# Kernel optimization log

Hardware: AMD Instinct MI355X
Metric: run time of the kernel (lower is better)

## Reference

```python
import jax, jax.numpy as jnp
import numpy as np

B, N, E, H = 1, 4096, 256, 4
D = E // H  # 64


def setup_inputs() -> dict:
    key = jax.random.key(0)
    ks = jax.random.split(key, 16)
    s = lambda fan_in: 1.0 / np.sqrt(fan_in)
    inp = {
        "x": jax.random.normal(ks[0], (B, N, E), dtype=jnp.float32),
        "encoding": jax.random.normal(ks[1], (2, 1, 1, N, D), dtype=jnp.float32),
        # Wqkv: Linear(E, 3E)
        "Wqkv_w": jax.random.uniform(ks[2], (3 * E, E), jnp.float32, -s(E), s(E)),
        "Wqkv_b": jax.random.uniform(ks[3], (3 * E,), jnp.float32, -s(E), s(E)),
        # out_proj: Linear(E, E)
        "out_w": jax.random.uniform(ks[4], (E, E), jnp.float32, -s(E), s(E)),
        "out_b": jax.random.uniform(ks[5], (E,), jnp.float32, -s(E), s(E)),
        # ffn[0]: Linear(2E, 2E)
        "ffn1_w": jax.random.uniform(ks[6], (2 * E, 2 * E), jnp.float32, -s(2 * E), s(2 * E)),
        "ffn1_b": jax.random.uniform(ks[7], (2 * E,), jnp.float32, -s(2 * E), s(2 * E)),
        # ffn[1]: LayerNorm(2E)
        "ln_g": jnp.ones((2 * E,), jnp.float32),
        "ln_b": jnp.zeros((2 * E,), jnp.float32),
        # ffn[3]: Linear(2E, E)
        "ffn2_w": jax.random.uniform(ks[8], (E, 2 * E), jnp.float32, -s(2 * E), s(2 * E)),
        "ffn2_b": jax.random.uniform(ks[9], (E,), jnp.float32, -s(2 * E), s(2 * E)),
    }
    return inp


def _rotate_half(t):
    # t: (B, H, N, D) -> pairwise rotate along last dim
    t2 = t.reshape(B, H, -1, D // 2, 2)
    t2 = jnp.stack((-t2[..., 1], t2[..., 0]), axis=-1)
    return t2.reshape(B, H, -1, D)


def _layernorm(x, g, b, eps=1e-5):
    mu = jnp.mean(x, axis=-1, keepdims=True)
    var = jnp.mean(jnp.square(x - mu), axis=-1, keepdims=True)
    return (x - mu) * jax.lax.rsqrt(var + eps) * g + b


def reference(x, encoding, Wqkv_w, Wqkv_b, out_w, out_b,
              ffn1_w, ffn1_b, ln_g, ln_b, ffn2_w, ffn2_b):
    # fused QKV projection; last dim layout is (H, D, 3)
    qkv = x @ Wqkv_w.T + Wqkv_b                       # (B, N, 3E)
    qkv = qkv.reshape(B, N, H, D, 3).transpose(0, 2, 1, 3, 4)  # (B, H, N, D, 3)
    q, k, v = qkv[..., 0], qkv[..., 1], qkv[..., 2]
    # cached rotary embedding: t*cos + rotate_half(t)*sin
    q = q * encoding[0] + _rotate_half(q) * encoding[1]
    k = k * encoding[0] + _rotate_half(k) * encoding[1]
    # scaled dot-product attention (no mask)
    scores = jnp.einsum("bhqd,bhkd->bhqk", q, k) / np.sqrt(D).astype(np.float32)
    probs = jax.nn.softmax(scores, axis=-1)
    ctx = jnp.einsum("bhqk,bhkd->bhqd", probs, v)     # (B, H, N, D)
    ctx = ctx.transpose(0, 2, 1, 3).reshape(B, N, E)
    message = ctx @ out_w.T + out_b
    # concat-FFN with residual
    h = jnp.concatenate((x, message), axis=-1)        # (B, N, 2E)
    h = h @ ffn1_w.T + ffn1_b
    h = _layernorm(h, ln_g, ln_b)
    h = jax.nn.gelu(h, approximate=False)
    h = h @ ffn2_w.T + ffn2_b
    return x + h
```

## Files before the change

### kernel.cpp

```cpp
#include <hip/hip_runtime.h>
#include <math.h>

#define NTOK 4096
#define EMB  256
#define NH   4
#define HD   64

typedef unsigned short u16;
typedef __attribute__((ext_vector_type(8))) __bf16 bf16x8;
typedef __attribute__((ext_vector_type(4))) float f32x4;

__device__ __forceinline__ u16 f2bf(float f) {
    union { float f; unsigned u; } v; v.f = f;
    unsigned b = v.u;
    b += 0x7FFFu + ((b >> 16) & 1u);
    return (u16)(b >> 16);
}
__device__ __forceinline__ float bf2f(u16 u) {
    union { unsigned u; float f; } v; v.u = ((unsigned)u) << 16;
    return v.f;
}

__global__ __launch_bounds__(256) void w4cast(
    const float4* __restrict__ w0, const float4* __restrict__ w1,
    const float4* __restrict__ w2, const float4* __restrict__ w3,
    u16* __restrict__ dst)
{
    const int f = blockIdx.x * 256 + threadIdx.x;
    float4 v;
    if      (f <  49152) v = w0[f];
    else if (f <  65536) v = w1[f - 49152];
    else if (f < 131072) v = w2[f - 65536];
    else                 v = w3[f - 131072];
    uint2 o;
    o.x = (unsigned)f2bf(v.x) | ((unsigned)f2bf(v.y) << 16);
    o.y = (unsigned)f2bf(v.z) | ((unsigned)f2bf(v.w) << 16);
    *(uint2*)(dst + (size_t)f * 4) = o;
}

__global__ __launch_bounds__(256) void xcast(
    const float4* __restrict__ x4, u16* __restrict__ xb, u16* __restrict__ catb)
{
    const int f = blockIdx.x * 256 + threadIdx.x;
    float4 v = x4[f];
    uint2 o;
    o.x = (unsigned)f2bf(v.x) | ((unsigned)f2bf(v.y) << 16);
    o.y = (unsigned)f2bf(v.z) | ((unsigned)f2bf(v.w) << 16);
    *(uint2*)(xb + (size_t)f * 4) = o;
    const int row = f >> 6, c = (f & 63) * 4;
    *(uint2*)(catb + (size_t)row * 512 + c) = o;
}

__global__ __launch_bounds__(256) void gemm_bf16_abt(
    const u16* __restrict__ A,
    const u16* __restrict__ B,
    const float* __restrict__ bias,
    const float* __restrict__ resid, int ldr,
    float* __restrict__ Cf, u16* __restrict__ Cb, int ldc, int K)
{
    const int t = threadIdx.x, w = t >> 6, l = t & 63;
    const int lg = l >> 4, li = l & 15;
    const int row0 = blockIdx.y * 64 + w * 16;
    const int col0 = blockIdx.x * 64;

    f32x4 acc[4];
    #pragma unroll
    for (int nb = 0; nb < 4; ++nb) acc[nb] = (f32x4){0.f, 0.f, 0.f, 0.f};

    const u16* Ap = A + (size_t)(row0 + li) * K + lg * 8;
    const u16* Bp = B + (size_t)(col0 + li) * K + lg * 8;

    #pragma unroll 2
    for (int k0 = 0; k0 < K; k0 += 32) {
        bf16x8 a = *(const bf16x8*)(Ap + k0);
        #pragma unroll
        for (int nb = 0; nb < 4; ++nb) {
            bf16x8 b = *(const bf16x8*)(Bp + (size_t)nb * 16 * K + k0);
            acc[nb] = __builtin_amdgcn_mfma_f32_16x16x32_bf16(a, b, acc[nb], 0, 0, 0);
        }
    }

    #pragma unroll
    for (int nb = 0; nb < 4; ++nb) {
        const int col = col0 + nb * 16 + li;
        const float bs = bias[col];
        #pragma unroll
        for (int p = 0; p < 4; ++p) {
            const int row = row0 + lg * 4 + p;
            float v = acc[nb][p] + bs;
            if (resid) v += resid[(size_t)row * ldr + col];
            if (Cf) Cf[(size_t)row * ldc + col] = v;
            else    Cb[(size_t)row * ldc + col] = f2bf(v);
        }
    }
}

__global__ __launch_bounds__(256) void rope_qk(
    const u16* __restrict__ qkvb, const float* __restrict__ enc,
    unsigned* __restrict__ Qb, unsigned* __restrict__ Kb)
{
    const int gid = blockIdx.x * 256 + threadIdx.x;
    const int h   = gid >> 17;
    const int rem = gid & (NTOK * 32 - 1);
    const int n   = rem >> 5;
    const int p   = rem & 31;
    const int d0  = p * 2;

    const u16* base = qkvb + (size_t)n * 768 + h * 192 + d0 * 3;
    const float q0v = bf2f(base[0]), k0 = bf2f(base[1]);
    const float q1  = bf2f(base[3]), k1 = bf2f(base[4]);

    float2 c01 = *(const float2*)(enc + (size_t)n * 64 + d0);
    float2 s01 = *(const float2*)(enc + (size_t)NTOK * 64 + (size_t)n * 64 + d0);

    const float qo0 = (q0v * c01.x - q1 * s01.x) * 0.125f;
    const float qo1 = (q1 * c01.y + q0v * s01.y) * 0.125f;
    const float ko0 = k0 * c01.x - k1 * s01.x;
    const float ko1 = k1 * c01.y + k0 * s01.y;

    const size_t oidx = ((size_t)(h * NTOK + n) << 5) + p;
    Qb[oidx] = (unsigned)f2bf(qo0) | ((unsigned)f2bf(qo1) << 16);
    Kb[oidx] = (unsigned)f2bf(ko0) | ((unsigned)f2bf(ko1) << 16);
}

__global__ __launch_bounds__(256) void v_transpose(
    const u16* __restrict__ qkvb, u16* __restrict__ Vt)
{
    const int h  = blockIdx.x >> 6;
    const int nt = blockIdx.x & 63;
    const int t  = threadIdx.x;
    const int d  = t & 63;
    const int nc = t >> 6;

    __align__(16) u16 us[16];
    #pragma unroll
    for (int i = 0; i < 16; ++i) {
        const int n = nt * 64 + nc * 16 + i;
        us[i] = qkvb[(size_t)n * 768 + h * 192 + d * 3 + 2];
    }
    u16* dst = Vt + ((size_t)(h * 64 + d) << 12) + nt * 64 + nc * 16;
    *(uint4*)(dst)     = *(uint4*)(us);
    *(uint4*)(dst + 8) = *(uint4*)(us + 8);
}

__global__ __launch_bounds__(512, 2) void flash_attn_mfma8(
    const u16* __restrict__ Qb, const u16* __restrict__ Kb,
    const u16* __restrict__ Vt, u16* __restrict__ ctxb)
{
    __shared__ char  Plds[8 * 4096];
    __shared__ float Obuf[64 * 64];
    __shared__ float Mbuf[64], Lbuf[64];

    const int t  = threadIdx.x;
    const int w  = t >> 6;
    const int l  = t & 63;
    const int lg = l >> 4, li = l & 15;
    const int wq = w >> 2, wk = w & 3;
    const int h  = blockIdx.y;
    const int q0 = blockIdx.x * 64;

    char* Pw = Plds + w * 4096;

    bf16x8 QA[2][2];
    #pragma unroll
    for (int Mb = 0; Mb < 2; ++Mb)
        #pragma unroll
        for (int kh = 0; kh < 2; ++kh)
            QA[Mb][kh] = *(const bf16x8*)(Qb +
                ((size_t)(h * NTOK + q0 + wq * 32 + Mb * 16 + li) << 6) + kh * 32 + lg * 8);

    f32x4 OA[2][4];
    float mrun[2][4], lrun[2][4];
    #pragma unroll
    for (int Mb = 0; Mb < 2; ++Mb) {
        #pragma unroll
        for (int p = 0; p < 4; ++p) { mrun[Mb][p] = -1e30f; lrun[Mb][p] = 0.f; }
        #pragma unroll
        for (int db = 0; db < 4; ++db) OA[Mb][db] = (f32x4){0.f, 0.f, 0.f, 0.f};
    }

    for (int it = 0; it < 16; ++it) {
        const int kt = (wk << 10) + (it << 6);

        bf16x8 KB[4][2], VB[4][2];
        #pragma unroll
        for (int kb = 0; kb < 4; ++kb)
            #pragma unroll
            for (int kh = 0; kh < 2; ++kh)
                KB[kb][kh] = *(const bf16x8*)(Kb +
                    ((size_t)(h * NTOK + kt + kb * 16 + li) << 6) + kh * 32 + lg * 8);
        #pragma unroll
        for (int db = 0; db < 4; ++db)
            #pragma unroll
            for (int kh = 0; kh < 2; ++kh)
                VB[db][kh] = *(const bf16x8*)(Vt +
                    ((size_t)(h * 64 + db * 16 + li) << 12) + kt + kh * 32 + lg * 8);

        f32x4 SA[2][4];
        #pragma unroll
        for (int Mb = 0; Mb < 2; ++Mb)
            #pragma unroll
            for (int kb = 0; kb < 4; ++kb) {
                f32x4 z = (f32x4){0.f, 0.f, 0.f, 0.f};
                z = __builtin_amdgcn_mfma_f32_16x16x32_bf16(QA[Mb][0], KB[kb][0], z, 0, 0, 0);
                SA[Mb][kb] = __builtin_amdgcn_mfma_f32_16x16x32_bf16(QA[Mb][1], KB[kb][1], z, 0, 0, 0);
            }

        #pragma unroll
        for (int Mb = 0; Mb < 2; ++Mb)
            #pragma unroll
            for (int p = 0; p < 4; ++p) {
                float mx = fmaxf(fmaxf(SA[Mb][0][p], SA[Mb][1][p]),
                                 fmaxf(SA[Mb][2][p], SA[Mb][3][p]));
                #pragma unroll
                for (int sh = 1; sh < 16; sh <<= 1)
                    mx = fmaxf(mx, __shfl_xor(mx, sh));
                const float mo = mrun[Mb][p];
                const float mn = fmaxf(mo, mx);
                const float corr = __expf(mo - mn);
                mrun[Mb][p] = mn;
                float pv[4], ps = 0.f;
                #pragma unroll
                for (int kb = 0; kb < 4; ++kb) {
                    pv[kb] = __expf(SA[Mb][kb][p] - mn);
                    ps += pv[kb];
                }
                #pragma unroll
                for (int sh = 1; sh < 16; sh <<= 1) ps += __shfl_xor(ps, sh);
                lrun[Mb][p] = lrun[Mb][p] * corr + ps;
                #pragma unroll
                for (int db = 0; db < 4; ++db) OA[Mb][db][p] *= corr;

                const int ql = Mb * 16 + lg * 4 + p;
                #pragma unroll
                for (int kb = 0; kb < 4; ++kb) {
                    const int kl = kb * 16 + li;
                    *(u16*)(Pw + ql * 128 + ((kl * 2) ^ ((ql & 7) << 4))) = f2bf(pv[kb]);
                }
            }

        #pragma unroll
        for (int Mb = 0; Mb < 2; ++Mb)
            #pragma unroll
            for (int kh = 0; kh < 2; ++kh) {
                const int ql = Mb * 16 + li;
                bf16x8 PA = *(const bf16x8*)(Pw + ql * 128 +
                                ((kh * 64 + lg * 16) ^ ((ql & 7) << 4)));
                #pragma unroll
                for (int db = 0; db < 4; ++db)
                    OA[Mb][db] = __builtin_amdgcn_mfma_f32_16x16x32_bf16(
                        PA, VB[db][kh], OA[Mb][db], 0, 0, 0);
            }
    }

    if (wk == 0) {
        #pragma unroll
        for (int Mb = 0; Mb < 2; ++Mb)
            #pragma unroll
            for (int p = 0; p < 4; ++p) {
                const int q = wq * 32 + Mb * 16 + lg * 4 + p;
                #pragma unroll
                for (int db = 0; db < 4; ++db)
                    Obuf[q * 64 + db * 16 + li] = OA[Mb][db][p];
                if (li == 0) { Mbuf[q] = mrun[Mb][p]; Lbuf[q] = lrun[Mb][p]; }
            }
    }
    #pragma unroll
    for (int wv = 1; wv < 4; ++wv) {
        __syncthreads();
        if (wk == wv) {
            #pragma unroll
            for (int Mb = 0; Mb < 2; ++Mb)
                #pragma unroll
                for (int p = 0; p < 4; ++p) {
                    const int q = wq * 32 + Mb * 16 + lg * 4 + p;
                    const float Mo = Mbuf[q], Lo = Lbuf[q];
                    const float mn = fmaxf(Mo, mrun[Mb][p]);
                    const float a  = __expf(Mo - mn);
                    const float b  = __expf(mrun[Mb][p] - mn);
                    #pragma unroll
                    for (int db = 0; db < 4; ++db) {
                        const int idx = q * 64 + db * 16 + li;
                        Obuf[idx] = Obuf[idx] * a + OA[Mb][db][p] * b;
                    }
                    if (li == 0) { Mbuf[q] = mn; Lbuf[q] = Lo * a + lrun[Mb][p] * b; }
                }
        }
    }
    __syncthreads();

    {
        const int q = t >> 3, dc = (t & 7) * 8;
        const float rl = 1.f / Lbuf[q];
        uint4 ov;
        unsigned* op = (unsigned*)&ov;
        #pragma unroll
        for (int i = 0; i < 8; i += 2)
            op[i >> 1] = (unsigned)f2bf(Obuf[q * 64 + dc + i] * rl) |
                         ((unsigned)f2bf(Obuf[q * 64 + dc + i + 1] * rl) << 16);
        *(uint4*)(ctxb + (size_t)(q0 + q) * EMB + h * 64 + dc) = ov;
    }
}

__global__ __launch_bounds__(256) void ln_gelu(
    const float* __restrict__ h1, const float* __restrict__ g,
    const float* __restrict__ b, u16* __restrict__ h2b)
{
    __shared__ float red[8];
    const int row = blockIdx.x, t = threadIdx.x;
    const float v0 = h1[(size_t)row * 512 + t];
    const float v1 = h1[(size_t)row * 512 + 256 + t];

    float s = v0 + v1;
    #pragma unroll
    for (int w = 1; w < 64; w <<= 1) s += __shfl_xor(s, w);
    if ((t & 63) == 0) red[t >> 6] = s;
    __syncthreads();
    const float mu = (red[0] + red[1] + red[2] + red[3]) * (1.f / 512.f);

    const float d0 = v0 - mu, d1 = v1 - mu;
    float vs = d0 * d0 + d1 * d1;
    #pragma unroll
    for (int w = 1; w < 64; w <<= 1) vs += __shfl_xor(vs, w);
    if ((t & 63) == 0) red[4 + (t >> 6)] = vs;
    __syncthreads();
    const float var  = (red[4] + red[5] + red[6] + red[7]) * (1.f / 512.f);
    const float rstd = rsqrtf(var + 1e-5f);

    const float y0 = d0 * rstd * g[t] + b[t];
    const float y1 = d1 * rstd * g[t + 256] + b[t + 256];
    const float o0 = 0.5f * y0 * (1.f + erff(y0 * 0.70710678118654752f));
    const float o1 = 0.5f * y1 * (1.f + erff(y1 * 0.70710678118654752f));
    h2b[(size_t)row * 512 + t]       = f2bf(o0);
    h2b[(size_t)row * 512 + 256 + t] = f2bf(o1);
}

extern "C" void kernel_launch(void* const* d_in, const int* in_sizes, int n_in,
                              void* d_out, int out_size, void* d_ws, size_t ws_size,
                              hipStream_t stream)
{
    const float* x      = (const float*)d_in[0];
    const float* enc    = (const float*)d_in[1];
    const float* Wqkv_w = (const float*)d_in[2];
    const float* Wqkv_b = (const float*)d_in[3];
    const float* out_w  = (const float*)d_in[4];
    const float* out_b  = (const float*)d_in[5];
    const float* ffn1_w = (const float*)d_in[6];
    const float* ffn1_b = (const float*)d_in[7];
    const float* ln_g   = (const float*)d_in[8];
    const float* ln_b   = (const float*)d_in[9];
    const float* ffn2_w = (const float*)d_in[10];
    const float* ffn2_b = (const float*)d_in[11];
    float* out = (float*)d_out;
    float* ws  = (float*)d_ws;

    u16*   catb = (u16*)(ws);
    u16*   wb   = (u16*)(ws + 1048576);
    u16*   Qb   = (u16*)(ws + 1376256);
    u16*   Kb   = (u16*)(ws + 1900544);
    u16*   Vt   = (u16*)(ws + 2424832);
    u16*   ctxb = (u16*)(ws + 2949120);
    u16*   qkvb = (u16*)(ws + 3473408);
    float* h1   = ws + 3473408;
    u16*   xb   = (u16*)(ws + 5570560);
    u16*   h2b  = (u16*)(ws + 5570560);

    u16* Wqkvb = wb;
    u16* outwb = wb + 196608;
    u16* ffn1b = wb + 262144;
    u16* ffn2b = wb + 524288;

    w4cast<<<640, 256, 0, stream>>>((const float4*)Wqkv_w, (const float4*)out_w,
                                    (const float4*)ffn1_w, (const float4*)ffn2_w, wb);
    xcast<<<1024, 256, 0, stream>>>((const float4*)x, xb, catb);
    gemm_bf16_abt<<<dim3(12, 64), 256, 0, stream>>>(xb, Wqkvb, Wqkv_b,
                                                    nullptr, 0, nullptr, qkvb, 768, 256);
    rope_qk<<<2048, 256, 0, stream>>>(qkvb, enc, (unsigned*)Qb, (unsigned*)Kb);
    v_transpose<<<256, 256, 0, stream>>>(qkvb, Vt);
    flash_attn_mfma8<<<dim3(64, NH), 512, 0, stream>>>(Qb, Kb, Vt, ctxb);
    gemm_bf16_abt<<<dim3(4, 64), 256, 0, stream>>>(ctxb, outwb, out_b,
                                                   nullptr, 0, nullptr, catb + 256, 512, 256);
    gemm_bf16_abt<<<dim3(8, 64), 256, 0, stream>>>(catb, ffn1b, ffn1_b,
                                                   nullptr, 0, h1, nullptr, 512, 512);
    ln_gelu<<<4096, 256, 0, stream>>>(h1, ln_g, ln_b, h2b);
    gemm_bf16_abt<<<dim3(4, 64), 256, 0, stream>>>(h2b, ffn2b, ffn2_b,
                                                   x, 256, out, nullptr, 256, 512);
}
```

Baseline: 229.9 us.

## Fuse prep kernels, split attention keys across 8 waves, defer row-sum reduction

Merges the weight and input cast kernels into one launch, and merges RoPE with the V transpose, removing two launches. Flash attention now uses 32-query blocks with all 8 waves splitting the key range, so the grid doubles to 512 blocks for better CU occupancy. The per-iteration shuffle reduction of the softmax row sum is moved to a single reduction after the loop. In exchange, the cross-wave merge now runs 7 serialized LDS merge steps instead of 3, and each K/V tile is loaded by half as many query rows.

```diff
diff --git a/kernel.cpp b/kernel.cpp
--- a/kernel.cpp
+++ b/kernel.cpp
@@ -21,34 +21,34 @@
     return v.f;
 }
 
-__global__ __launch_bounds__(256) void w4cast(
+__global__ __launch_bounds__(256) void prep(
     const float4* __restrict__ w0, const float4* __restrict__ w1,
     const float4* __restrict__ w2, const float4* __restrict__ w3,
-    u16* __restrict__ dst)
-{
-    const int f = blockIdx.x * 256 + threadIdx.x;
-    float4 v;
-    if      (f <  49152) v = w0[f];
-    else if (f <  65536) v = w1[f - 49152];
-    else if (f < 131072) v = w2[f - 65536];
-    else                 v = w3[f - 131072];
-    uint2 o;
-    o.x = (unsigned)f2bf(v.x) | ((unsigned)f2bf(v.y) << 16);
-    o.y = (unsigned)f2bf(v.z) | ((unsigned)f2bf(v.w) << 16);
-    *(uint2*)(dst + (size_t)f * 4) = o;
-}
-
-__global__ __launch_bounds__(256) void xcast(
+    u16* __restrict__ wb,
     const float4* __restrict__ x4, u16* __restrict__ xb, u16* __restrict__ catb)
 {
-    const int f = blockIdx.x * 256 + threadIdx.x;
-    float4 v = x4[f];
-    uint2 o;
-    o.x = (unsigned)f2bf(v.x) | ((unsigned)f2bf(v.y) << 16);
-    o.y = (unsigned)f2bf(v.z) | ((unsigned)f2bf(v.w) << 16);
-    *(uint2*)(xb + (size_t)f * 4) = o;
-    const int row = f >> 6, c = (f & 63) * 4;
-    *(uint2*)(catb + (size_t)row * 512 + c) = o;
+    const int bid = blockIdx.x;
+    if (bid < 640) {
+        const int f = bid * 256 + threadIdx.x;
+        float4 v;
+        if      (f <  49152) v = w0[f];
+        else if (f <  65536) v = w1[f - 49152];
+        else if (f < 131072) v = w2[f - 65536];
+        else                 v = w3[f - 131072];
+        uint2 o;
+        o.x = (unsigned)f2bf(v.x) | ((unsigned)f2bf(v.y) << 16);
+        o.y = (unsigned)f2bf(v.z) | ((unsigned)f2bf(v.w) << 16);
+        *(uint2*)(wb + (size_t)f * 4) = o;
+    } else {
+        const int f = (bid - 640) * 256 + threadIdx.x;
+        float4 v = x4[f];
+        uint2 o;
+        o.x = (unsigned)f2bf(v.x) | ((unsigned)f2bf(v.y) << 16);
+        o.y = (unsigned)f2bf(v.z) | ((unsigned)f2bf(v.w) << 16);
+        *(uint2*)(xb + (size_t)f * 4) = o;
+        const int row = f >> 6, c = (f & 63) * 4;
+        *(uint2*)(catb + (size_t)row * 512 + c) = o;
+    }
 }
 
 __global__ __launch_bounds__(256) void gemm_bf16_abt(
@@ -95,71 +95,70 @@
     }
 }
 
-__global__ __launch_bounds__(256) void rope_qk(
+__global__ __launch_bounds__(256) void qkv_post(
     const u16* __restrict__ qkvb, const float* __restrict__ enc,
-    unsigned* __restrict__ Qb, unsigned* __restrict__ Kb)
-{
-    const int gid = blockIdx.x * 256 + threadIdx.x;
-    const int h   = gid >> 17;
-    const int rem = gid & (NTOK * 32 - 1);
-    const int n   = rem >> 5;
-    const int p   = rem & 31;
-    const int d0  = p * 2;
-
-    const u16* base = qkvb + (size_t)n * 768 + h * 192 + d0 * 3;
-    const float q0v = bf2f(base[0]), k0 = bf2f(base[1]);
-    const float q1  = bf2f(base[3]), k1 = bf2f(base[4]);
-
-    float2 c01 = *(const float2*)(enc + (size_t)n * 64 + d0);
-    float2 s01 = *(const float2*)(enc + (size_t)NTOK * 64 + (size_t)n * 64 + d0);
-
-    const float qo0 = (q0v * c01.x - q1 * s01.x) * 0.125f;
-    const float qo1 = (q1 * c01.y + q0v * s01.y) * 0.125f;
-    const float ko0 = k0 * c01.x - k1 * s01.x;
-    const float ko1 = k1 * c01.y + k0 * s01.y;
-
-    const size_t oidx = ((size_t)(h * NTOK + n) << 5) + p;
-    Qb[oidx] = (unsigned)f2bf(qo0) | ((unsigned)f2bf(qo1) << 16);
-    Kb[oidx] = (unsigned)f2bf(ko0) | ((unsigned)f2bf(ko1) << 16);
-}
-
-__global__ __launch_bounds__(256) void v_transpose(
-    const u16* __restrict__ qkvb, u16* __restrict__ Vt)
-{
-    const int h  = blockIdx.x >> 6;
-    const int nt = blockIdx.x & 63;
-    const int t  = threadIdx.x;
-    const int d  = t & 63;
-    const int nc = t >> 6;
-
-    __align__(16) u16 us[16];
-    #pragma unroll
-    for (int i = 0; i < 16; ++i) {
-        const int n = nt * 64 + nc * 16 + i;
-        us[i] = qkvb[(size_t)n * 768 + h * 192 + d * 3 + 2];
-    }
-    u16* dst = Vt + ((size_t)(h * 64 + d) << 12) + nt * 64 + nc * 16;
-    *(uint4*)(dst)     = *(uint4*)(us);
-    *(uint4*)(dst + 8) = *(uint4*)(us + 8);
-}
-
-__global__ __launch_bounds__(512, 2) void flash_attn_mfma8(
+    unsigned* __restrict__ Qb, unsigned* __restrict__ Kb, u16* __restrict__ Vt)
+{
+    const int bid = blockIdx.x;
+    if (bid < 2048) {
+        const int gid = bid * 256 + threadIdx.x;
+        const int h   = gid >> 17;
+        const int rem = gid & (NTOK * 32 - 1);
+        const int n   = rem >> 5;
+        const int p   = rem & 31;
+        const int d0  = p * 2;
+
+        const u16* base = qkvb + (size_t)n * 768 + h * 192 + d0 * 3;
+        const float q0v = bf2f(base[0]), k0 = bf2f(base[1]);
+        const float q1  = bf2f(base[3]), k1 = bf2f(base[4]);
+
+        float2 c01 = *(const float2*)(enc + (size_t)n * 64 + d0);
+        float2 s01 = *(const float2*)(enc + (size_t)NTOK * 64 + (size_t)n * 64 + d0);
+
+        const float qo0 = (q0v * c01.x - q1 * s01.x) * 0.125f;
+        const float qo1 = (q1 * c01.y + q0v * s01.y) * 0.125f;
+        const float ko0 = k0 * c01.x - k1 * s01.x;
+        const float ko1 = k1 * c01.y + k0 * s01.y;
+
+        const size_t oidx = ((size_t)(h * NTOK + n) << 5) + p;
+        Qb[oidx] = (unsigned)f2bf(qo0) | ((unsigned)f2bf(qo1) << 16);
+        Kb[oidx] = (unsigned)f2bf(ko0) | ((unsigned)f2bf(ko1) << 16);
+    } else {
+        const int vb = bid - 2048;
+        const int h  = vb >> 6;
+        const int nt = vb & 63;
+        const int t  = threadIdx.x;
+        const int d  = t & 63;
+        const int nc = t >> 6;
+
+        __align__(16) u16 us[16];
+        #pragma unroll
+        for (int i = 0; i < 16; ++i) {
+            const int n = nt * 64 + nc * 16 + i;
+            us[i] = qkvb[(size_t)n * 768 + h * 192 + d * 3 + 2];
+        }
+        u16* dst = Vt + ((size_t)(h * 64 + d) << 12) + nt * 64 + nc * 16;
+        *(uint4*)(dst)     = *(uint4*)(us);
+        *(uint4*)(dst + 8) = *(uint4*)(us + 8);
+    }
+}
+
+__global__ __launch_bounds__(512, 2) void flash_attn_v3(
     const u16* __restrict__ Qb, const u16* __restrict__ Kb,
     const u16* __restrict__ Vt, u16* __restrict__ ctxb)
 {
     __shared__ char  Plds[8 * 4096];
-    __shared__ float Obuf[64 * 64];
-    __shared__ float Mbuf[64], Lbuf[64];
+    __shared__ float Obuf[32 * 64];
+    __shared__ float Mbuf[32], Lbuf[32];
 
     const int t  = threadIdx.x;
-    const int w  = t >> 6;
+    const int wk = t >> 6;
     const int l  = t & 63;
     const int lg = l >> 4, li = l & 15;
-    const int wq = w >> 2, wk = w & 3;
     const int h  = blockIdx.y;
-    const int q0 = blockIdx.x * 64;
-
-    char* Pw = Plds + w * 4096;
+    const int q0 = blockIdx.x * 32;
+
+    char* Pw = Plds + wk * 4096;
 
     bf16x8 QA[2][2];
     #pragma unroll
@@ -167,7 +166,7 @@
         #pragma unroll
         for (int kh = 0; kh < 2; ++kh)
             QA[Mb][kh] = *(const bf16x8*)(Qb +
-                ((size_t)(h * NTOK + q0 + wq * 32 + Mb * 16 + li) << 6) + kh * 32 + lg * 8);
+                ((size_t)(h * NTOK + q0 + Mb * 16 + li) << 6) + kh * 32 + lg * 8);
 
     f32x4 OA[2][4];
     float mrun[2][4], lrun[2][4];
@@ -179,8 +178,8 @@
         for (int db = 0; db < 4; ++db) OA[Mb][db] = (f32x4){0.f, 0.f, 0.f, 0.f};
     }
 
-    for (int it = 0; it < 16; ++it) {
-        const int kt = (wk << 10) + (it << 6);
+    for (int it = 0; it < 8; ++it) {
+        const int kt = (wk << 9) + (it << 6);
 
         bf16x8 KB[4][2], VB[4][2];
         #pragma unroll
@@ -225,8 +224,6 @@
                     pv[kb] = __expf(SA[Mb][kb][p] - mn);
                     ps += pv[kb];
                 }
-                #pragma unroll
-                for (int sh = 1; sh < 16; sh <<= 1) ps += __shfl_xor(ps, sh);
                 lrun[Mb][p] = lrun[Mb][p] * corr + ps;
                 #pragma unroll
                 for (int db = 0; db < 4; ++db) OA[Mb][db][p] *= corr;
@@ -253,12 +250,22 @@
             }
     }
 
+    #pragma unroll
+    for (int Mb = 0; Mb < 2; ++Mb)
+        #pragma unroll
+        for (int p = 0; p < 4; ++p) {
+            float ps = lrun[Mb][p];
+            #pragma unroll
+            for (int sh = 1; sh < 16; sh <<= 1) ps += __shfl_xor(ps, sh);
+            lrun[Mb][p] = ps;
+        }
+
     if (wk == 0) {
         #pragma unroll
         for (int Mb = 0; Mb < 2; ++Mb)
             #pragma unroll
             for (int p = 0; p < 4; ++p) {
-                const int q = wq * 32 + Mb * 16 + lg * 4 + p;
+                const int q = Mb * 16 + lg * 4 + p;
                 #pragma unroll
                 for (int db = 0; db < 4; ++db)
                     Obuf[q * 64 + db * 16 + li] = OA[Mb][db][p];
@@ -266,14 +273,14 @@
             }
     }
     #pragma unroll
-    for (int wv = 1; wv < 4; ++wv) {
+    for (int wv = 1; wv < 8; ++wv) {
         __syncthreads();
         if (wk == wv) {
             #pragma unroll
             for (int Mb = 0; Mb < 2; ++Mb)
                 #pragma unroll
                 for (int p = 0; p < 4; ++p) {
-                    const int q = wq * 32 + Mb * 16 + lg * 4 + p;
+                    const int q = Mb * 16 + lg * 4 + p;
                     const float Mo = Mbuf[q], Lo = Lbuf[q];
                     const float mn = fmaxf(Mo, mrun[Mb][p]);
                     const float a  = __expf(Mo - mn);
@@ -290,15 +297,14 @@
     __syncthreads();
 
     {
-        const int q = t >> 3, dc = (t & 7) * 8;
+        const int q = t >> 4, dc = (t & 15) * 4;
         const float rl = 1.f / Lbuf[q];
-        uint4 ov;
-        unsigned* op = (unsigned*)&ov;
-        #pragma unroll
-        for (int i = 0; i < 8; i += 2)
-            op[i >> 1] = (unsigned)f2bf(Obuf[q * 64 + dc + i] * rl) |
-                         ((unsigned)f2bf(Obuf[q * 64 + dc + i + 1] * rl) << 16);
-        *(uint4*)(ctxb + (size_t)(q0 + q) * EMB + h * 64 + dc) = ov;
+        uint2 ov;
+        ov.x = (unsigned)f2bf(Obuf[q * 64 + dc + 0] * rl) |
+               ((unsigned)f2bf(Obuf[q * 64 + dc + 1] * rl) << 16);
+        ov.y = (unsigned)f2bf(Obuf[q * 64 + dc + 2] * rl) |
+               ((unsigned)f2bf(Obuf[q * 64 + dc + 3] * rl) << 16);
+        *(uint2*)(ctxb + (size_t)(q0 + q) * EMB + h * 64 + dc) = ov;
     }
 }
 
@@ -370,14 +376,13 @@
     u16* ffn1b = wb + 262144;
     u16* ffn2b = wb + 524288;
 
-    w4cast<<<640, 256, 0, stream>>>((const float4*)Wqkv_w, (const float4*)out_w,
-                                    (const float4*)ffn1_w, (const float4*)ffn2_w, wb);
-    xcast<<<1024, 256, 0, stream>>>((const float4*)x, xb, catb);
+    prep<<<1664, 256, 0, stream>>>((const float4*)Wqkv_w, (const float4*)out_w,
+                                   (const float4*)ffn1_w, (const float4*)ffn2_w, wb,
+                                   (const float4*)x, xb, catb);
     gemm_bf16_abt<<<dim3(12, 64), 256, 0, stream>>>(xb, Wqkvb, Wqkv_b,
                                                     nullptr, 0, nullptr, qkvb, 768, 256);
-    rope_qk<<<2048, 256, 0, stream>>>(qkvb, enc, (unsigned*)Qb, (unsigned*)Kb);
-    v_transpose<<<256, 256, 0, stream>>>(qkvb, Vt);
-    flash_attn_mfma8<<<dim3(64, NH), 512, 0, stream>>>(Qb, Kb, Vt, ctxb);
+    qkv_post<<<2304, 256, 0, stream>>>(qkvb, enc, (unsigned*)Qb, (unsigned*)Kb, Vt);
+    flash_attn_v3<<<dim3(128, NH), 512, 0, stream>>>(Qb, Kb, Vt, ctxb);
     gemm_bf16_abt<<<dim3(4, 64), 256, 0, stream>>>(ctxb, outwb, out_b,
                                                    nullptr, 0, nullptr, catb + 256, 512, 256);
     gemm_bf16_abt<<<dim3(8, 64), 256, 0, stream>>>(catb, ffn1b, ffn1_b,
```

Result: slower. 239.5 us (+4.2%).
